# Optimization experiments

Hardware: AMD Instinct MI355X
Metric: run time of the kernel (lower is better)

## Reference

```python
import jax, jax.numpy as jnp
import numpy as np

B, S, D, H, DH, W, V, K = 2, 4096, 768, 12, 64, 128, 50265, 128
NEG = -1e9


def _ln(x, g, b, eps=1e-5):
    m = jnp.mean(x, axis=-1, keepdims=True)
    v = jnp.var(x, axis=-1, keepdims=True)
    return (x - m) * jax.lax.rsqrt(v + eps) * g + b


def _split_heads(x):  # [B,S,D] -> [B,H,S,DH]
    return x.reshape(B, S, H, DH).transpose(0, 2, 1, 3)


def _windows(xc):  # [B,H,C,W,DH] -> [B,H,C,3W,DH] (prev/self/next chunk)
    xp = jnp.pad(xc, ((0, 0), (0, 0), (1, 1), (0, 0), (0, 0)))
    return jnp.concatenate([xp[:, :, :-2], xp[:, :, 1:-1], xp[:, :, 2:]], axis=3)


def _forward(sentences, start_pieces, end_pieces, labels,
             emb, pos, ln0_g, ln0_b, wq, bq, wk, bk, wv, bv, wo, bo,
             ln1_g, ln1_b, w1, b1, w2, b2, ln2_g, ln2_b, exemplars):
    C = S // W
    scale = 1.0 / np.sqrt(DH)
    am = sentences != 1  # pad token id is 1 (mask = sentence_tokens != 1)
    gidx = jnp.concatenate([start_pieces, end_pieces], axis=1)  # [B,2] global tokens
    G = gidx.shape[1]

    # embeddings
    x = _ln(emb[sentences] + pos[None], ln0_g, ln0_b)  # [B,S,D]

    # --- Longformer layer: sliding-window + global attention ---
    q = _split_heads(x @ wq + bq)
    k = _split_heads(x @ wk + bk)
    v = _split_heads(x @ wv + bv)

    qc = q.reshape(B, H, C, W, DH)
    kw = _windows(k.reshape(B, H, C, W, DH))  # [B,H,C,3W,DH]
    vw = _windows(v.reshape(B, H, C, W, DH))

    # banded local scores
    sb = jnp.einsum('bhcqd,bhckd->bhcqk', qc, kw) * scale  # [B,H,C,W,3W]
    qi = jnp.arange(W)[:, None]
    kj = jnp.arange(3 * W)[None, :]
    band = jnp.abs(kj - W - qi) <= W  # [W,3W]
    amc = jnp.pad(am.reshape(B, C, W), ((0, 0), (1, 1), (0, 0)))
    amw = jnp.concatenate([amc[:, :-2], amc[:, 1:-1], amc[:, 2:]], axis=2)  # [B,C,3W]
    mask = band[None, None, None] & amw[:, None, :, None, :]
    sb = jnp.where(mask, sb, NEG).reshape(B, H, S, 3 * W)

    # every token also attends to the G global tokens
    gk = jnp.take_along_axis(k, gidx[:, None, :, None], axis=2)  # [B,H,G,DH]
    gv = jnp.take_along_axis(v, gidx[:, None, :, None], axis=2)
    sg = jnp.einsum('bhsd,bhgd->bhsg', q, gk) * scale  # [B,H,S,G]

    p = jax.nn.softmax(jnp.concatenate([sb, sg], axis=-1), axis=-1)
    pb = p[..., :3 * W].reshape(B, H, C, W, 3 * W)
    pg = p[..., 3 * W:]
    o = jnp.einsum('bhcqk,bhckd->bhcqd', pb, vw).reshape(B, H, S, DH)
    o = o + jnp.einsum('bhsg,bhgd->bhsd', pg, gv)

    # global query tokens attend to everything
    qg = jnp.take_along_axis(q, gidx[:, None, :, None], axis=2)  # [B,H,G,DH]
    sgq = jnp.einsum('bhgd,bhsd->bhgs', qg, k) * scale
    sgq = jnp.where(am[:, None, None, :], sgq, NEG)
    og = jnp.einsum('bhgs,bhsd->bhgd', jax.nn.softmax(sgq, axis=-1), v)

    o = o.transpose(0, 2, 1, 3).reshape(B, S, D)
    og = og.transpose(0, 2, 1, 3).reshape(B, G, D)
    o = o.at[jnp.arange(B)[:, None], gidx].set(og)

    x = _ln(x + (o @ wo + bo), ln1_g, ln1_b)
    ff = jax.nn.gelu(x @ w1 + b1, approximate=False) @ w2 + b2
    h = _ln(x + ff, ln2_g, ln2_b)  # last_hidden_state

    # mention reps: gather start & end piece vectors, concat -> [B, 2D]
    sv = jnp.take_along_axis(h, start_pieces[:, :, None], axis=1)[:, 0]
    ev = jnp.take_along_axis(h, end_pieces[:, :, None], axis=1)[:, 0]
    mention = jnp.concatenate([sv, ev], axis=-1)  # [B, 1536]

    logits = mention @ exemplars.T  # [B, K]
    logp = jax.nn.log_softmax(logits, axis=-1)
    loss = -jnp.sum(jnp.take_along_axis(logp, labels[:, None], axis=1))
    return logits, loss


def setup_inputs() -> dict:
    key = jax.random.key(0)
    ks = jax.random.split(key, 16)
    f = lambda k, s: (jax.random.normal(k, s, dtype=jnp.float32) * 0.02)
    return {
        'sentences': jax.random.randint(ks[0], (B, S), 0, V, dtype=jnp.int32),
        'start_pieces': jax.random.randint(ks[1], (B, 1), 0, S, dtype=jnp.int32),
        'end_pieces': jax.random.randint(ks[2], (B, 1), 0, S, dtype=jnp.int32),
        'labels': jax.random.randint(ks[3], (B,), 0, K, dtype=jnp.int32),
        'emb': f(ks[4], (V, D)), 'pos': f(ks[5], (S, D)),
        'ln0_g': jnp.ones(D), 'ln0_b': jnp.zeros(D),
        'wq': f(ks[6], (D, D)), 'bq': jnp.zeros(D),
        'wk': f(ks[7], (D, D)), 'bk': jnp.zeros(D),
        'wv': f(ks[8], (D, D)), 'bv': jnp.zeros(D),
        'wo': f(ks[9], (D, D)), 'bo': jnp.zeros(D),
        'ln1_g': jnp.ones(D), 'ln1_b': jnp.zeros(D),
        'w1': f(ks[10], (D, 4 * D)), 'b1': jnp.zeros(4 * D),
        'w2': f(ks[11], (4 * D, D)), 'b2': jnp.zeros(D),
        'ln2_g': jnp.ones(D), 'ln2_b': jnp.zeros(D),
        'exemplars': f(ks[12], (K, 2 * D)),
    }


def reference(sentences, start_pieces, end_pieces, labels,
              emb, pos, ln0_g, ln0_b, wq, bq, wk, bk, wv, bv, wo, bo,
              ln1_g, ln1_b, w1, b1, w2, b2, ln2_g, ln2_b, exemplars):
    return _forward(sentences, start_pieces, end_pieces, labels,
                    emb, pos, ln0_g, ln0_b, wq, bq, wk, bk, wv, bv, wo, bo,
                    ln1_g, ln1_b, w1, b1, w2, b2, ln2_g, ln2_b, exemplars)
```

## Files before the change

### kernel.cpp

```cpp
#include <hip/hip_runtime.h>

typedef unsigned short u16;
typedef unsigned int   u32;
typedef __attribute__((ext_vector_type(8))) short bf16x8;
typedef __attribute__((ext_vector_type(4))) float f32x4;

#define BB 2
#define SS 4096
#define DD 768
#define HH 12
#define FF 3072
#define NTOK 8192

#define GLDS16(gp, lp) __builtin_amdgcn_global_load_lds(                      \
    (const __attribute__((address_space(1))) u32*)(gp),                       \
    (__attribute__((address_space(3))) u32*)(lp), 16, 0, 0)

__device__ __forceinline__ float bf2f(u16 u) {
  u32 x = ((u32)u) << 16;
  return __uint_as_float(x);
}
__device__ __forceinline__ u16 f2bf(float f) {
  u32 x = __float_as_uint(f);
  x = x + 0x7FFFu + ((x >> 16) & 1u);
  return (u16)(x >> 16);
}
__device__ __forceinline__ float gelu_f(float v) {
  return 0.5f * v * (1.0f + erff(v * 0.70710678118654752f));
}

template<bool MAXOP>
__device__ __forceinline__ float blk_reduce(float v, float* sbuf) {
  #pragma unroll
  for (int o = 32; o > 0; o >>= 1) {
    float t = __shfl_xor(v, o, 64);
    v = MAXOP ? fmaxf(v, t) : (v + t);
  }
  int wave = threadIdx.x >> 6;
  int nw = blockDim.x >> 6;
  __syncthreads();
  if ((threadIdx.x & 63) == 0) sbuf[wave] = v;
  __syncthreads();
  float r = sbuf[0];
  for (int i = 1; i < nw; i++) r = MAXOP ? fmaxf(r, sbuf[i]) : (r + sbuf[i]);
  return r;
}

__global__ __launch_bounds__(256) void transcvt2(const float* __restrict__ wk,
    const float* __restrict__ wv, u16* __restrict__ wkT, u16* __restrict__ wvT) {
  const float* W = blockIdx.z ? wv : wk;
  u16* WT = blockIdx.z ? wvT : wkT;
  __shared__ float t[32][33];
  int n0 = blockIdx.x * 32, k0 = blockIdx.y * 32;
  int tx = threadIdx.x & 31, ty = threadIdx.x >> 5;
  #pragma unroll
  for (int i = 0; i < 32; i += 8)
    t[ty + i][tx] = W[(size_t)(k0 + ty + i) * DD + n0 + tx];
  __syncthreads();
  #pragma unroll
  for (int i = 0; i < 32; i += 8)
    WT[(size_t)(n0 + ty + i) * DD + k0 + tx] = f2bf(t[tx][ty + i]);
}

__global__ void seed_k(const int* sp, const int* ep, const float* bq, const float* bo,
                       const float* b1, const float* b2,
                       float* qg, float* oa, float* f1, float* f2, int* gidx) {
  int tid = threadIdx.x;
  if (tid < 4) {
    int b = tid >> 1;
    int s = (tid & 1) ? ep[b] : sp[b];
    gidx[tid] = b * SS + s;
  }
  for (int i = tid; i < DD; i += 256) {
    float vq = bq[i], vo = bo[i], v2 = b2[i];
    #pragma unroll
    for (int r = 0; r < 4; r++) {
      qg[r * DD + i] = vq; oa[r * DD + i] = vo; f2[r * DD + i] = v2;
    }
  }
  for (int i = tid; i < FF; i += 256) {
    float v1 = b1[i];
    #pragma unroll
    for (int r = 0; r < 4; r++) f1[r * FF + i] = v1;
  }
}

__global__ __launch_bounds__(192) void embed_ln_k(const int* __restrict__ sent,
    const float* __restrict__ emb, const float* __restrict__ pos,
    const float* __restrict__ g, const float* __restrict__ be, u16* __restrict__ xout) {
  __shared__ float sbuf[8];
  int tok = blockIdx.x;
  int s = tok & (SS - 1);
  int row = sent[tok];
  int tid = threadIdx.x;
  float4 e = *(const float4*)(emb + (size_t)row * DD + tid * 4);
  float4 p = *(const float4*)(pos + (size_t)s * DD + tid * 4);
  float v0 = e.x + p.x, v1 = e.y + p.y, v2 = e.z + p.z, v3 = e.w + p.w;
  float sum = v0 + v1 + v2 + v3;
  float sq  = v0 * v0 + v1 * v1 + v2 * v2 + v3 * v3;
  sum = blk_reduce<false>(sum, sbuf);
  sq  = blk_reduce<false>(sq, sbuf);
  float mean = sum * (1.f / DD);
  float var  = sq * (1.f / DD) - mean * mean;
  float rstd = rsqrtf(var + 1e-5f);
  float4 gg = *(const float4*)(g + tid * 4);
  float4 bb = *(const float4*)(be + tid * 4);
  float o0 = (v0 - mean) * rstd * gg.x + bb.x;
  float o1 = (v1 - mean) * rstd * gg.y + bb.y;
  float o2 = (v2 - mean) * rstd * gg.z + bb.z;
  float o3 = (v3 - mean) * rstd * gg.w + bb.w;
  u32 lo = (u32)f2bf(o0) | ((u32)f2bf(o1) << 16);
  u32 hi = (u32)f2bf(o2) | ((u32)f2bf(o3) << 16);
  uint2 st; st.x = lo; st.y = hi;
  *(uint2*)(xout + (size_t)tok * DD + tid * 4) = st;
}

__global__ __launch_bounds__(256) void gemm_kv(const u16* __restrict__ A,
    const u16* __restrict__ wkT, const u16* __restrict__ wvT,
    const float* __restrict__ bkp, const float* __restrict__ bvp,
    u16* __restrict__ kb, u16* __restrict__ vb) {
  const int K = DD, N = DD;
  __shared__ u16 As[128 * 32];
  __shared__ u16 Bs[128 * 32];
  int which = blockIdx.y >= 6;
  int m0 = blockIdx.x * 128;
  int n0 = (blockIdx.y - (which ? 6 : 0)) * 128;
  const u16* Bt = which ? wvT : wkT;
  const float* bias = which ? bvp : bkp;
  u16* C = which ? vb : kb;
  int tid = threadIdx.x;
  int lane = tid & 63, wave = tid >> 6;
  int wr = wave >> 1, wc = wave & 1;
  f32x4 acc[4][4] = {};
  int ch0 = wave * 64 + lane;
  int r0 = ch0 >> 2, su0 = ch0 & 3;
  int ch1 = 256 + ch0;
  int r1 = ch1 >> 2, su1 = ch1 & 3;
  const u16* a0p = A  + (size_t)(m0 + r0) * K + su0 * 8;
  const u16* a1p = A  + (size_t)(m0 + r1) * K + su1 * 8;
  const u16* b0p = Bt + (size_t)(n0 + r0) * K + su0 * 8;
  const u16* b1p = Bt + (size_t)(n0 + r1) * K + su1 * 8;
  u16* AsW0 = As + (size_t)(wave * 64) * 8;
  u16* AsW1 = As + (size_t)(256 + wave * 64) * 8;
  u16* BsW0 = Bs + (size_t)(wave * 64) * 8;
  u16* BsW1 = Bs + (size_t)(256 + wave * 64) * 8;
  int fr = lane & 15, fk = (lane >> 4) * 8;
  for (int k0 = 0; k0 < K; k0 += 32) {
    GLDS16(a0p + k0, AsW0);
    GLDS16(a1p + k0, AsW1);
    GLDS16(b0p + k0, BsW0);
    GLDS16(b1p + k0, BsW1);
    __syncthreads();
    bf16x8 af[4], bfr[4];
    #pragma unroll
    for (int i = 0; i < 4; i++)
      af[i] = *(const bf16x8*)(As + ((wr * 64 + i * 16 + fr) << 5) + fk);
    #pragma unroll
    for (int j = 0; j < 4; j++)
      bfr[j] = *(const bf16x8*)(Bs + ((wc * 64 + j * 16 + fr) << 5) + fk);
    #pragma unroll
    for (int i = 0; i < 4; i++)
      #pragma unroll
      for (int j = 0; j < 4; j++)
        acc[i][j] = __builtin_amdgcn_mfma_f32_16x16x32_bf16(af[i], bfr[j], acc[i][j], 0, 0, 0);
    __syncthreads();
  }
  int cr = (lane >> 4) * 4;
  int cc = lane & 15;
  #pragma unroll
  for (int i = 0; i < 4; i++) {
    #pragma unroll
    for (int j = 0; j < 4; j++) {
      int col = n0 + wc * 64 + j * 16 + cc;
      float bvv = bias[col];
      int rowb = m0 + wr * 64 + i * 16 + cr;
      #pragma unroll
      for (int r = 0; r < 4; r++) {
        float v = acc[i][j][r] + bvv;
        C[(size_t)(rowb + r) * N + col] = f2bf(v);
      }
    }
  }
}

__global__ __launch_bounds__(256) void matvec4(const float* __restrict__ W,
    const float* __restrict__ inF, const u16* __restrict__ inB, const int* __restrict__ gidx,
    float* __restrict__ acc, int K, int N, int kchunk, int mode) {
  __shared__ float s_in[4 * 256];
  int n = blockIdx.x * 256 + threadIdx.x;
  int k0 = blockIdx.y * kchunk;
  for (int idx = threadIdx.x; idx < 4 * kchunk; idx += 256) {
    int r = idx / kchunk, kk = idx - r * kchunk;
    float vv;
    if (mode == 1) vv = bf2f(inB[(size_t)gidx[r] * K + k0 + kk]);
    else vv = inF[(size_t)r * K + k0 + kk];
    if (mode == 2) vv = gelu_f(vv);
    s_in[r * 256 + kk] = vv;
  }
  __syncthreads();
  float a0 = 0.f, a1 = 0.f, a2 = 0.f, a3 = 0.f;
  for (int kk = 0; kk < kchunk; kk++) {
    float w = W[(size_t)(k0 + kk) * N + n];
    a0 += s_in[kk] * w;
    a1 += s_in[256 + kk] * w;
    a2 += s_in[512 + kk] * w;
    a3 += s_in[768 + kk] * w;
  }
  atomicAdd(&acc[n], a0);
  atomicAdd(&acc[N + n], a1);
  atomicAdd(&acc[2 * N + n], a2);
  atomicAdd(&acc[3 * N + n], a3);
}

__global__ __launch_bounds__(256) void gattn_part(const u16* __restrict__ kb,
    const u16* __restrict__ vb, const float* __restrict__ qg, const int* __restrict__ sent,
    float* __restrict__ part) {
  int sc = blockIdx.x, h = blockIdx.y, bg = blockIdx.z;
  int b = bg >> 1;
  __shared__ float pbuf[256];
  __shared__ float ovs[32][64];
  __shared__ float sbuf[8];
  int tid = threadIdx.x;
  int rsub = tid >> 3, csub = tid & 7;
  float qr[8];
  #pragma unroll
  for (int j = 0; j < 8; j++) qr[j] = qg[bg * DD + h * 64 + csub * 8 + j];
  size_t kbase = ((size_t)b * SS + sc * 256) * DD + h * 64 + csub * 8;
  #pragma unroll
  for (int pass = 0; pass < 8; pass++) {
    int rowi = pass * 32 + rsub;
    uint4 u = *(const uint4*)(kb + kbase + (size_t)rowi * DD);
    u32 vals[4] = {u.x, u.y, u.z, u.w};
    float dot = 0.f;
    #pragma unroll
    for (int t = 0; t < 4; t++) {
      dot += qr[t * 2]     * __uint_as_float(vals[t] << 16);
      dot += qr[t * 2 + 1] * __uint_as_float(vals[t] & 0xFFFF0000u);
    }
    dot += __shfl_xor(dot, 1, 64);
    dot += __shfl_xor(dot, 2, 64);
    dot += __shfl_xor(dot, 4, 64);
    if (csub == 0) pbuf[rowi] = dot;
  }
  __syncthreads();
  float score = (sent[b * SS + sc * 256 + tid] != 1) ? pbuf[tid] * 0.125f : -1e9f;
  float m = blk_reduce<true>(score, sbuf);
  float p = expf(score - m);
  float psum = blk_reduce<false>(p, sbuf);
  pbuf[tid] = p;
  __syncthreads();
  float a[8] = {0.f, 0.f, 0.f, 0.f, 0.f, 0.f, 0.f, 0.f};
  #pragma unroll
  for (int pass = 0; pass < 8; pass++) {
    int rowi = pass * 32 + rsub;
    uint4 u = *(const uint4*)(vb + kbase + (size_t)rowi * DD);
    u32 vals[4] = {u.x, u.y, u.z, u.w};
    float pw = pbuf[rowi];
    #pragma unroll
    for (int t = 0; t < 4; t++) {
      a[t * 2]     += pw * __uint_as_float(vals[t] << 16);
      a[t * 2 + 1] += pw * __uint_as_float(vals[t] & 0xFFFF0000u);
    }
  }
  #pragma unroll
  for (int j = 0; j < 8; j++) ovs[rsub][csub * 8 + j] = a[j];
  __syncthreads();
  float* pp = part + (((size_t)bg * HH + h) * 16 + sc) * 66;
  if (tid == 0) { pp[0] = m; pp[1] = psum; }
  if (tid < 64) {
    float o = 0.f;
    #pragma unroll
    for (int g2 = 0; g2 < 32; g2++) o += ovs[g2][tid];
    pp[2 + tid] = o;
  }
}

__global__ __launch_bounds__(256) void matvec_wo(const float* __restrict__ W,
    const float* __restrict__ part, float* __restrict__ acc) {
  __shared__ float s_in[4][64];
  int h = blockIdx.y;
  int tid = threadIdx.x;
  int bg = tid >> 6, d = tid & 63;
  const float* pp = part + (((size_t)bg * HH + h) * 16) * 66;
  float M = -1e30f;
  for (int c = 0; c < 16; c++) M = fmaxf(M, pp[c * 66]);
  float Ssum = 0.f, o = 0.f;
  for (int c = 0; c < 16; c++) {
    float e = expf(pp[c * 66] - M);
    Ssum += pp[c * 66 + 1] * e;
    o += pp[c * 66 + 2 + d] * e;
  }
  s_in[bg][d] = o / Ssum;
  __syncthreads();
  int n = blockIdx.x * 256 + tid;
  int k0 = h * 64;
  float a0 = 0.f, a1 = 0.f, a2 = 0.f, a3 = 0.f;
  for (int kk = 0; kk < 64; kk++) {
    float w = W[(size_t)(k0 + kk) * DD + n];
    a0 += s_in[0][kk] * w;
    a1 += s_in[1][kk] * w;
    a2 += s_in[2][kk] * w;
    a3 += s_in[3][kk] * w;
  }
  atomicAdd(&acc[n], a0);
  atomicAdd(&acc[DD + n], a1);
  atomicAdd(&acc[2 * DD + n], a2);
  atomicAdd(&acc[3 * DD + n], a3);
}

__global__ __launch_bounds__(256) void ln4_k(const u16* __restrict__ xb, const int* __restrict__ gidx,
    const float* __restrict__ in1f, const float* __restrict__ in2,
    const float* __restrict__ g, const float* __restrict__ be, float* __restrict__ outp) {
  __shared__ float sbuf[8];
  int r = blockIdx.x;
  float v[3];
  float sum = 0.f, sq = 0.f;
  #pragma unroll
  for (int i = 0; i < 3; i++) {
    int d = threadIdx.x + i * 256;
    float t;
    if (xb) t = bf2f(xb[(size_t)gidx[r] * DD + d]);
    else    t = in1f[r * DD + d];
    t += in2[r * DD + d];
    v[i] = t; sum += t; sq += t * t;
  }
  sum = blk_reduce<false>(sum, sbuf);
  sq  = blk_reduce<false>(sq, sbuf);
  float mean = sum * (1.f / DD);
  float var  = sq * (1.f / DD) - mean * mean;
  float rstd = rsqrtf(var + 1e-5f);
  #pragma unroll
  for (int i = 0; i < 3; i++) {
    int d = threadIdx.x + i * 256;
    outp[r * DD + d] = (v[i] - mean) * rstd * g[d] + be[d];
  }
}

__global__ __launch_bounds__(256) void logits_k(const float* __restrict__ hws,
    const float* __restrict__ ex, float* __restrict__ out) {
  __shared__ float sbuf[8];
  int j = blockIdx.x;
  const float* er = ex + (size_t)j * 1536;
  float d0 = 0.f, d1 = 0.f;
  for (int c = threadIdx.x; c < 768; c += 256) {
    float e0 = er[c], e1 = er[768 + c];
    d0 += hws[c] * e0 + hws[768 + c] * e1;
    d1 += hws[1536 + c] * e0 + hws[2304 + c] * e1;
  }
  d0 = blk_reduce<false>(d0, sbuf);
  d1 = blk_reduce<false>(d1, sbuf);
  if (threadIdx.x == 0) { out[j] = d0; out[128 + j] = d1; }
}

__global__ __launch_bounds__(128) void loss_k(const float* __restrict__ lg,
    const int* __restrict__ labels, float* __restrict__ out) {
  __shared__ float sbuf[8];
  int tid = threadIdx.x;
  float v0 = lg[tid], v1 = lg[128 + tid];
  float m0 = blk_reduce<true>(v0, sbuf);
  float m1 = blk_reduce<true>(v1, sbuf);
  float s0 = blk_reduce<false>(expf(v0 - m0), sbuf);
  float s1 = blk_reduce<false>(expf(v1 - m1), sbuf);
  if (tid == 0) {
    float lp0 = lg[labels[0]] - m0 - logf(s0);
    float lp1 = lg[128 + labels[1]] - m1 - logf(s1);
    out[256] = -(lp0 + lp1);
  }
}

extern "C" void kernel_launch(void* const* d_in, const int* in_sizes, int n_in,
                              void* d_out, int out_size, void* d_ws, size_t ws_size,
                              hipStream_t stream) {
  const int*   sent = (const int*)d_in[0];
  const int*   sp   = (const int*)d_in[1];
  const int*   ep   = (const int*)d_in[2];
  const int*   lab  = (const int*)d_in[3];
  const float* emb  = (const float*)d_in[4];
  const float* pos  = (const float*)d_in[5];
  const float* ln0g = (const float*)d_in[6];
  const float* ln0b = (const float*)d_in[7];
  const float* wq   = (const float*)d_in[8];
  const float* bq   = (const float*)d_in[9];
  const float* wk   = (const float*)d_in[10];
  const float* bk   = (const float*)d_in[11];
  const float* wv   = (const float*)d_in[12];
  const float* bv   = (const float*)d_in[13];
  const float* wo   = (const float*)d_in[14];
  const float* bo   = (const float*)d_in[15];
  const float* ln1g = (const float*)d_in[16];
  const float* ln1b = (const float*)d_in[17];
  const float* w1   = (const float*)d_in[18];
  const float* b1   = (const float*)d_in[19];
  const float* w2   = (const float*)d_in[20];
  const float* b2   = (const float*)d_in[21];
  const float* ln2g = (const float*)d_in[22];
  const float* ln2b = (const float*)d_in[23];
  const float* ex   = (const float*)d_in[24];
  float* out = (float*)d_out;

  char* basep = (char*)d_ws;
  size_t off = 0;
  auto alloc = [&](size_t bytes) -> void* {
    void* p = basep + off;
    off = (off + bytes + 255) & ~(size_t)255;
    return p;
  };
  u16*   xb   = (u16*)alloc((size_t)NTOK * DD * 2);
  u16*   kb   = (u16*)alloc((size_t)NTOK * DD * 2);
  u16*   vb   = (u16*)alloc((size_t)NTOK * DD * 2);
  u16*   wkT  = (u16*)alloc((size_t)DD * DD * 2);
  u16*   wvT  = (u16*)alloc((size_t)DD * DD * 2);
  float* qg   = (float*)alloc(4 * DD * 4);
  float* oacc = (float*)alloc(4 * DD * 4);
  float* x1   = (float*)alloc(4 * DD * 4);
  float* f1a  = (float*)alloc(4 * FF * 4);
  float* f2a  = (float*)alloc(4 * DD * 4);
  float* hws  = (float*)alloc(4 * DD * 4);
  float* part = (float*)alloc((size_t)4 * HH * 16 * 66 * 4);
  int*   gidx = (int*)alloc(64);

  transcvt2<<<dim3(24, 24, 2), 256, 0, stream>>>(wk, wv, wkT, wvT);
  seed_k<<<1, 256, 0, stream>>>(sp, ep, bq, bo, b1, b2, qg, oacc, f1a, f2a, gidx);
  embed_ln_k<<<NTOK, 192, 0, stream>>>(sent, emb, pos, ln0g, ln0b, xb);
  gemm_kv<<<dim3(64, 12), 256, 0, stream>>>(xb, wkT, wvT, bk, bv, kb, vb);
  matvec4<<<dim3(3, 12), 256, 0, stream>>>(wq, nullptr, xb, gidx, qg, DD, DD, 64, 1);
  gattn_part<<<dim3(16, HH, 4), 256, 0, stream>>>(kb, vb, qg, sent, part);
  matvec_wo<<<dim3(3, 12), 256, 0, stream>>>(wo, part, oacc);
  ln4_k<<<4, 256, 0, stream>>>(xb, gidx, nullptr, oacc, ln1g, ln1b, x1);
  matvec4<<<dim3(12, 12), 256, 0, stream>>>(w1, x1, nullptr, nullptr, f1a, DD, FF, 64, 0);
  matvec4<<<dim3(3, 24), 256, 0, stream>>>(w2, f1a, nullptr, nullptr, f2a, FF, DD, 128, 2);
  ln4_k<<<4, 256, 0, stream>>>(nullptr, nullptr, x1, f2a, ln2g, ln2b, hws);
  logits_k<<<128, 256, 0, stream>>>(hws, ex, out);
  loss_k<<<1, 128, 0, stream>>>(out, lab, out);
}
```

Baseline: 112.3 us.

## Fuse tail matvecs into cooperative kernel and merge small launches

Folds the seed kernel into the weight transpose kernel and the Wq matvec into the K/V GEMM launch, with an XCD-aware remapping of block ids. The attention-partials kernel now handles both global queries of a batch in one block, so each K/V chunk is read once instead of twice. The whole tail (Wo, LN1, FFN1, FFN2, LN2, logits, loss) becomes one cooperative kernel separated by grid syncs. This removes many small launches and their gaps, at the cost of grid-sync overhead and a fixed 192-block grid.

Measured after the change: 335.5 us. 199% more time.

```diff
diff --git a/kernel.cpp b/kernel.cpp
--- a/kernel.cpp
+++ b/kernel.cpp
@@ -1,4 +1,7 @@
 #include <hip/hip_runtime.h>
+#include <hip/hip_cooperative_groups.h>
+
+namespace cg = cooperative_groups;
 
 typedef unsigned short u16;
 typedef unsigned int   u32;
@@ -47,12 +50,35 @@
 }
 
 __global__ __launch_bounds__(256) void transcvt2(const float* __restrict__ wk,
-    const float* __restrict__ wv, u16* __restrict__ wkT, u16* __restrict__ wvT) {
+    const float* __restrict__ wv, u16* __restrict__ wkT, u16* __restrict__ wvT,
+    const int* sp, const int* ep, const float* bq, const float* bo,
+    const float* b1, const float* b2,
+    float* qg, float* oa, float* f1, float* f2, int* gidx) {
+  int tid = threadIdx.x;
+  if (blockIdx.x == 0 && blockIdx.y == 0 && blockIdx.z == 0) {
+    if (tid < 4) {
+      int b = tid >> 1;
+      int s = (tid & 1) ? ep[b] : sp[b];
+      gidx[tid] = b * SS + s;
+    }
+    for (int i = tid; i < DD; i += 256) {
+      float vq = bq[i], vo = bo[i], v2 = b2[i];
+      #pragma unroll
+      for (int r = 0; r < 4; r++) {
+        qg[r * DD + i] = vq; oa[r * DD + i] = vo; f2[r * DD + i] = v2;
+      }
+    }
+    for (int i = tid; i < FF; i += 256) {
+      float v1 = b1[i];
+      #pragma unroll
+      for (int r = 0; r < 4; r++) f1[r * FF + i] = v1;
+    }
+  }
   const float* W = blockIdx.z ? wv : wk;
   u16* WT = blockIdx.z ? wvT : wkT;
   __shared__ float t[32][33];
   int n0 = blockIdx.x * 32, k0 = blockIdx.y * 32;
-  int tx = threadIdx.x & 31, ty = threadIdx.x >> 5;
+  int tx = tid & 31, ty = tid >> 5;
   #pragma unroll
   for (int i = 0; i < 32; i += 8)
     t[ty + i][tx] = W[(size_t)(k0 + ty + i) * DD + n0 + tx];
@@ -60,29 +86,6 @@
   #pragma unroll
   for (int i = 0; i < 32; i += 8)
     WT[(size_t)(n0 + ty + i) * DD + k0 + tx] = f2bf(t[tx][ty + i]);
-}
-
-__global__ void seed_k(const int* sp, const int* ep, const float* bq, const float* bo,
-                       const float* b1, const float* b2,
-                       float* qg, float* oa, float* f1, float* f2, int* gidx) {
-  int tid = threadIdx.x;
-  if (tid < 4) {
-    int b = tid >> 1;
-    int s = (tid & 1) ? ep[b] : sp[b];
-    gidx[tid] = b * SS + s;
-  }
-  for (int i = tid; i < DD; i += 256) {
-    float vq = bq[i], vo = bo[i], v2 = b2[i];
-    #pragma unroll
-    for (int r = 0; r < 4; r++) {
-      qg[r * DD + i] = vq; oa[r * DD + i] = vo; f2[r * DD + i] = v2;
-    }
-  }
-  for (int i = tid; i < FF; i += 256) {
-    float v1 = b1[i];
-    #pragma unroll
-    for (int r = 0; r < 4; r++) f1[r * FF + i] = v1;
-  }
 }
 
 __global__ __launch_bounds__(192) void embed_ln_k(const int* __restrict__ sent,
@@ -118,17 +121,48 @@
 __global__ __launch_bounds__(256) void gemm_kv(const u16* __restrict__ A,
     const u16* __restrict__ wkT, const u16* __restrict__ wvT,
     const float* __restrict__ bkp, const float* __restrict__ bvp,
-    u16* __restrict__ kb, u16* __restrict__ vb) {
-  const int K = DD, N = DD;
+    u16* __restrict__ kb, u16* __restrict__ vb,
+    const float* __restrict__ wqw, const int* __restrict__ gidx,
+    float* __restrict__ qg) {
   __shared__ u16 As[128 * 32];
   __shared__ u16 Bs[128 * 32];
-  int which = blockIdx.y >= 6;
-  int m0 = blockIdx.x * 128;
-  int n0 = (blockIdx.y - (which ? 6 : 0)) * 128;
+  int orig = blockIdx.x;
+  int xcd = orig & 7, cidx = orig >> 3;
+  int wgid = (xcd < 4 ? xcd * 101 : 4 * 101 + (xcd - 4) * 100) + cidx;
+  int tid = threadIdx.x;
+  if (wgid >= 768) {
+    int wqi = wgid - 768;
+    int nc = wqi % 3, ky = wqi / 3;
+    float* s_in = (float*)As;
+    if (tid < 256) {
+      int rr = tid >> 6, kk = tid & 63;
+      s_in[tid] = bf2f(A[(size_t)gidx[rr] * DD + ky * 64 + kk]);
+    }
+    __syncthreads();
+    int n = nc * 256 + tid;
+    int k0 = ky * 64;
+    float a0 = 0.f, a1 = 0.f, a2 = 0.f, a3 = 0.f;
+    for (int kk = 0; kk < 64; kk++) {
+      float w = wqw[(size_t)(k0 + kk) * DD + n];
+      a0 += s_in[kk] * w;
+      a1 += s_in[64 + kk] * w;
+      a2 += s_in[128 + kk] * w;
+      a3 += s_in[192 + kk] * w;
+    }
+    atomicAdd(&qg[n], a0);
+    atomicAdd(&qg[DD + n], a1);
+    atomicAdd(&qg[2 * DD + n], a2);
+    atomicAdd(&qg[3 * DD + n], a3);
+    return;
+  }
+  const int K = DD, N = DD;
+  int mx = wgid / 12, t = wgid % 12;
+  int which = t >= 6;
+  int m0 = mx * 128;
+  int n0 = (t - (which ? 6 : 0)) * 128;
   const u16* Bt = which ? wvT : wkT;
   const float* bias = which ? bvp : bkp;
   u16* C = which ? vb : kb;
-  int tid = threadIdx.x;
   int lane = tid & 63, wave = tid >> 6;
   int wr = wave >> 1, wc = wave & 1;
   f32x4 acc[4][4] = {};
@@ -183,188 +217,251 @@
   }
 }
 
-__global__ __launch_bounds__(256) void matvec4(const float* __restrict__ W,
-    const float* __restrict__ inF, const u16* __restrict__ inB, const int* __restrict__ gidx,
-    float* __restrict__ acc, int K, int N, int kchunk, int mode) {
-  __shared__ float s_in[4 * 256];
-  int n = blockIdx.x * 256 + threadIdx.x;
-  int k0 = blockIdx.y * kchunk;
-  for (int idx = threadIdx.x; idx < 4 * kchunk; idx += 256) {
-    int r = idx / kchunk, kk = idx - r * kchunk;
-    float vv;
-    if (mode == 1) vv = bf2f(inB[(size_t)gidx[r] * K + k0 + kk]);
-    else vv = inF[(size_t)r * K + k0 + kk];
-    if (mode == 2) vv = gelu_f(vv);
-    s_in[r * 256 + kk] = vv;
-  }
-  __syncthreads();
-  float a0 = 0.f, a1 = 0.f, a2 = 0.f, a3 = 0.f;
-  for (int kk = 0; kk < kchunk; kk++) {
-    float w = W[(size_t)(k0 + kk) * N + n];
-    a0 += s_in[kk] * w;
-    a1 += s_in[256 + kk] * w;
-    a2 += s_in[512 + kk] * w;
-    a3 += s_in[768 + kk] * w;
-  }
-  atomicAdd(&acc[n], a0);
-  atomicAdd(&acc[N + n], a1);
-  atomicAdd(&acc[2 * N + n], a2);
-  atomicAdd(&acc[3 * N + n], a3);
-}
-
 __global__ __launch_bounds__(256) void gattn_part(const u16* __restrict__ kb,
     const u16* __restrict__ vb, const float* __restrict__ qg, const int* __restrict__ sent,
     float* __restrict__ part) {
-  int sc = blockIdx.x, h = blockIdx.y, bg = blockIdx.z;
-  int b = bg >> 1;
-  __shared__ float pbuf[256];
-  __shared__ float ovs[32][64];
+  int sc = blockIdx.x, h = blockIdx.y, b = blockIdx.z;
+  __shared__ float pbuf0[256], pbuf1[256];
+  __shared__ float ovs0[32][64], ovs1[32][64];
   __shared__ float sbuf[8];
   int tid = threadIdx.x;
   int rsub = tid >> 3, csub = tid & 7;
-  float qr[8];
-  #pragma unroll
-  for (int j = 0; j < 8; j++) qr[j] = qg[bg * DD + h * 64 + csub * 8 + j];
+  float qr0[8], qr1[8];
+  #pragma unroll
+  for (int j = 0; j < 8; j++) {
+    qr0[j] = qg[(2 * b) * DD + h * 64 + csub * 8 + j];
+    qr1[j] = qg[(2 * b + 1) * DD + h * 64 + csub * 8 + j];
+  }
   size_t kbase = ((size_t)b * SS + sc * 256) * DD + h * 64 + csub * 8;
   #pragma unroll
   for (int pass = 0; pass < 8; pass++) {
     int rowi = pass * 32 + rsub;
     uint4 u = *(const uint4*)(kb + kbase + (size_t)rowi * DD);
     u32 vals[4] = {u.x, u.y, u.z, u.w};
-    float dot = 0.f;
+    float d0 = 0.f, d1 = 0.f;
     #pragma unroll
     for (int t = 0; t < 4; t++) {
-      dot += qr[t * 2]     * __uint_as_float(vals[t] << 16);
-      dot += qr[t * 2 + 1] * __uint_as_float(vals[t] & 0xFFFF0000u);
-    }
-    dot += __shfl_xor(dot, 1, 64);
-    dot += __shfl_xor(dot, 2, 64);
-    dot += __shfl_xor(dot, 4, 64);
-    if (csub == 0) pbuf[rowi] = dot;
+      float lo = __uint_as_float(vals[t] << 16);
+      float hi = __uint_as_float(vals[t] & 0xFFFF0000u);
+      d0 += qr0[t * 2] * lo + qr0[t * 2 + 1] * hi;
+      d1 += qr1[t * 2] * lo + qr1[t * 2 + 1] * hi;
+    }
+    d0 += __shfl_xor(d0, 1, 64); d1 += __shfl_xor(d1, 1, 64);
+    d0 += __shfl_xor(d0, 2, 64); d1 += __shfl_xor(d1, 2, 64);
+    d0 += __shfl_xor(d0, 4, 64); d1 += __shfl_xor(d1, 4, 64);
+    if (csub == 0) { pbuf0[rowi] = d0; pbuf1[rowi] = d1; }
   }
   __syncthreads();
-  float score = (sent[b * SS + sc * 256 + tid] != 1) ? pbuf[tid] * 0.125f : -1e9f;
-  float m = blk_reduce<true>(score, sbuf);
-  float p = expf(score - m);
-  float psum = blk_reduce<false>(p, sbuf);
-  pbuf[tid] = p;
+  int ok = sent[b * SS + sc * 256 + tid] != 1;
+  float s0 = ok ? pbuf0[tid] * 0.125f : -1e9f;
+  float s1 = ok ? pbuf1[tid] * 0.125f : -1e9f;
+  float m0 = blk_reduce<true>(s0, sbuf);
+  float m1 = blk_reduce<true>(s1, sbuf);
+  float p0 = expf(s0 - m0);
+  float p1 = expf(s1 - m1);
+  float ps0 = blk_reduce<false>(p0, sbuf);
+  float ps1 = blk_reduce<false>(p1, sbuf);
+  pbuf0[tid] = p0;
+  pbuf1[tid] = p1;
   __syncthreads();
-  float a[8] = {0.f, 0.f, 0.f, 0.f, 0.f, 0.f, 0.f, 0.f};
+  float a0[8] = {0,0,0,0,0,0,0,0}, a1[8] = {0,0,0,0,0,0,0,0};
   #pragma unroll
   for (int pass = 0; pass < 8; pass++) {
     int rowi = pass * 32 + rsub;
     uint4 u = *(const uint4*)(vb + kbase + (size_t)rowi * DD);
     u32 vals[4] = {u.x, u.y, u.z, u.w};
-    float pw = pbuf[rowi];
+    float pw0 = pbuf0[rowi], pw1 = pbuf1[rowi];
     #pragma unroll
     for (int t = 0; t < 4; t++) {
-      a[t * 2]     += pw * __uint_as_float(vals[t] << 16);
-      a[t * 2 + 1] += pw * __uint_as_float(vals[t] & 0xFFFF0000u);
-    }
-  }
-  #pragma unroll
-  for (int j = 0; j < 8; j++) ovs[rsub][csub * 8 + j] = a[j];
+      float lo = __uint_as_float(vals[t] << 16);
+      float hi = __uint_as_float(vals[t] & 0xFFFF0000u);
+      a0[t * 2]     += pw0 * lo; a0[t * 2 + 1] += pw0 * hi;
+      a1[t * 2]     += pw1 * lo; a1[t * 2 + 1] += pw1 * hi;
+    }
+  }
+  #pragma unroll
+  for (int j = 0; j < 8; j++) {
+    ovs0[rsub][csub * 8 + j] = a0[j];
+    ovs1[rsub][csub * 8 + j] = a1[j];
+  }
   __syncthreads();
-  float* pp = part + (((size_t)bg * HH + h) * 16 + sc) * 66;
-  if (tid == 0) { pp[0] = m; pp[1] = psum; }
+  float* pp0 = part + (((size_t)(2 * b) * HH + h) * 16 + sc) * 66;
+  float* pp1 = part + (((size_t)(2 * b + 1) * HH + h) * 16 + sc) * 66;
+  if (tid == 0) { pp0[0] = m0; pp0[1] = ps0; pp1[0] = m1; pp1[1] = ps1; }
   if (tid < 64) {
-    float o = 0.f;
-    #pragma unroll
-    for (int g2 = 0; g2 < 32; g2++) o += ovs[g2][tid];
-    pp[2 + tid] = o;
-  }
-}
-
-__global__ __launch_bounds__(256) void matvec_wo(const float* __restrict__ W,
-    const float* __restrict__ part, float* __restrict__ acc) {
-  __shared__ float s_in[4][64];
-  int h = blockIdx.y;
-  int tid = threadIdx.x;
-  int bg = tid >> 6, d = tid & 63;
-  const float* pp = part + (((size_t)bg * HH + h) * 16) * 66;
-  float M = -1e30f;
-  for (int c = 0; c < 16; c++) M = fmaxf(M, pp[c * 66]);
-  float Ssum = 0.f, o = 0.f;
-  for (int c = 0; c < 16; c++) {
-    float e = expf(pp[c * 66] - M);
-    Ssum += pp[c * 66 + 1] * e;
-    o += pp[c * 66 + 2 + d] * e;
-  }
-  s_in[bg][d] = o / Ssum;
-  __syncthreads();
-  int n = blockIdx.x * 256 + tid;
-  int k0 = h * 64;
-  float a0 = 0.f, a1 = 0.f, a2 = 0.f, a3 = 0.f;
-  for (int kk = 0; kk < 64; kk++) {
-    float w = W[(size_t)(k0 + kk) * DD + n];
-    a0 += s_in[0][kk] * w;
-    a1 += s_in[1][kk] * w;
-    a2 += s_in[2][kk] * w;
-    a3 += s_in[3][kk] * w;
-  }
-  atomicAdd(&acc[n], a0);
-  atomicAdd(&acc[DD + n], a1);
-  atomicAdd(&acc[2 * DD + n], a2);
-  atomicAdd(&acc[3 * DD + n], a3);
-}
-
-__global__ __launch_bounds__(256) void ln4_k(const u16* __restrict__ xb, const int* __restrict__ gidx,
-    const float* __restrict__ in1f, const float* __restrict__ in2,
-    const float* __restrict__ g, const float* __restrict__ be, float* __restrict__ outp) {
+    float o0 = 0.f, o1 = 0.f;
+    #pragma unroll
+    for (int g2 = 0; g2 < 32; g2++) { o0 += ovs0[g2][tid]; o1 += ovs1[g2][tid]; }
+    pp0[2 + tid] = o0;
+    pp1[2 + tid] = o1;
+  }
+}
+
+struct TailArgs {
+  const float* part; const float* wo; float* oacc;
+  const u16* xb; const int* gidx;
+  const float* ln1g; const float* ln1b; float* x1;
+  const float* w1; float* f1a;
+  const float* w2; float* f2a;
+  const float* ln2g; const float* ln2b; float* hws;
+  const float* ex; float* out; const int* lab;
+};
+
+__global__ __launch_bounds__(256) void tail_k(TailArgs a) {
+  cg::grid_group grid = cg::this_grid();
+  int blk = blockIdx.x, tid = threadIdx.x;
   __shared__ float sbuf[8];
-  int r = blockIdx.x;
-  float v[3];
-  float sum = 0.f, sq = 0.f;
-  #pragma unroll
-  for (int i = 0; i < 3; i++) {
-    int d = threadIdx.x + i * 256;
-    float t;
-    if (xb) t = bf2f(xb[(size_t)gidx[r] * DD + d]);
-    else    t = in1f[r * DD + d];
-    t += in2[r * DD + d];
-    v[i] = t; sum += t; sq += t * t;
-  }
-  sum = blk_reduce<false>(sum, sbuf);
-  sq  = blk_reduce<false>(sq, sbuf);
-  float mean = sum * (1.f / DD);
-  float var  = sq * (1.f / DD) - mean * mean;
-  float rstd = rsqrtf(var + 1e-5f);
-  #pragma unroll
-  for (int i = 0; i < 3; i++) {
-    int d = threadIdx.x + i * 256;
-    outp[r * DD + d] = (v[i] - mean) * rstd * g[d] + be[d];
-  }
-}
-
-__global__ __launch_bounds__(256) void logits_k(const float* __restrict__ hws,
-    const float* __restrict__ ex, float* __restrict__ out) {
-  __shared__ float sbuf[8];
-  int j = blockIdx.x;
-  const float* er = ex + (size_t)j * 1536;
-  float d0 = 0.f, d1 = 0.f;
-  for (int c = threadIdx.x; c < 768; c += 256) {
-    float e0 = er[c], e1 = er[768 + c];
-    d0 += hws[c] * e0 + hws[768 + c] * e1;
-    d1 += hws[1536 + c] * e0 + hws[2304 + c] * e1;
-  }
-  d0 = blk_reduce<false>(d0, sbuf);
-  d1 = blk_reduce<false>(d1, sbuf);
-  if (threadIdx.x == 0) { out[j] = d0; out[128 + j] = d1; }
-}
-
-__global__ __launch_bounds__(128) void loss_k(const float* __restrict__ lg,
-    const int* __restrict__ labels, float* __restrict__ out) {
-  __shared__ float sbuf[8];
-  int tid = threadIdx.x;
-  float v0 = lg[tid], v1 = lg[128 + tid];
-  float m0 = blk_reduce<true>(v0, sbuf);
-  float m1 = blk_reduce<true>(v1, sbuf);
-  float s0 = blk_reduce<false>(expf(v0 - m0), sbuf);
-  float s1 = blk_reduce<false>(expf(v1 - m1), sbuf);
-  if (tid == 0) {
-    float lp0 = lg[labels[0]] - m0 - logf(s0);
-    float lp1 = lg[128 + labels[1]] - m1 - logf(s1);
-    out[256] = -(lp0 + lp1);
+  __shared__ float sm[4][64];
+  __shared__ float sin[192];
+  if (blk < 36) {
+    int nc = blk % 3, h = blk / 3;
+    int bg = tid >> 6, d = tid & 63;
+    const float* pp = a.part + ((size_t)(bg * HH + h) * 16) * 66;
+    float M = -1e30f;
+    for (int c = 0; c < 16; c++) M = fmaxf(M, pp[c * 66]);
+    float Ssum = 0.f, o = 0.f;
+    for (int c = 0; c < 16; c++) {
+      float e = expf(pp[c * 66] - M);
+      Ssum += pp[c * 66 + 1] * e;
+      o += pp[c * 66 + 2 + d] * e;
+    }
+    sm[bg][d] = o / Ssum;
+    __syncthreads();
+    int n = nc * 256 + tid;
+    float a0 = 0.f, a1 = 0.f, a2 = 0.f, a3 = 0.f;
+    for (int kk = 0; kk < 64; kk++) {
+      float w = a.wo[(size_t)(h * 64 + kk) * DD + n];
+      a0 += sm[0][kk] * w;
+      a1 += sm[1][kk] * w;
+      a2 += sm[2][kk] * w;
+      a3 += sm[3][kk] * w;
+    }
+    atomicAdd(&a.oacc[n], a0);
+    atomicAdd(&a.oacc[DD + n], a1);
+    atomicAdd(&a.oacc[2 * DD + n], a2);
+    atomicAdd(&a.oacc[3 * DD + n], a3);
+  }
+  __threadfence();
+  grid.sync();
+  if (blk < 4) {
+    float v[3]; float sum = 0.f, sq = 0.f;
+    #pragma unroll
+    for (int i = 0; i < 3; i++) {
+      int d = tid + i * 256;
+      float t = bf2f(a.xb[(size_t)a.gidx[blk] * DD + d]) + a.oacc[blk * DD + d];
+      v[i] = t; sum += t; sq += t * t;
+    }
+    sum = blk_reduce<false>(sum, sbuf);
+    sq  = blk_reduce<false>(sq, sbuf);
+    float mean = sum * (1.f / DD);
+    float rstd = rsqrtf(sq * (1.f / DD) - mean * mean + 1e-5f);
+    #pragma unroll
+    for (int i = 0; i < 3; i++) {
+      int d = tid + i * 256;
+      a.x1[blk * DD + d] = (v[i] - mean) * rstd * a.ln1g[d] + a.ln1b[d];
+    }
+  }
+  __threadfence();
+  grid.sync();
+  {
+    int nc = blk % 12, kc = blk / 12;
+    int k0 = kc * 48;
+    if (tid < 192) {
+      int rr = tid / 48, kk = tid - rr * 48;
+      sin[tid] = a.x1[rr * DD + k0 + kk];
+    }
+    __syncthreads();
+    int n = nc * 256 + tid;
+    float a0 = 0.f, a1 = 0.f, a2 = 0.f, a3 = 0.f;
+    for (int kk = 0; kk < 48; kk++) {
+      float w = a.w1[(size_t)(k0 + kk) * FF + n];
+      a0 += sin[kk] * w;
+      a1 += sin[48 + kk] * w;
+      a2 += sin[96 + kk] * w;
+      a3 += sin[144 + kk] * w;
+    }
+    atomicAdd(&a.f1a[n], a0);
+    atomicAdd(&a.f1a[FF + n], a1);
+    atomicAdd(&a.f1a[2 * FF + n], a2);
+    atomicAdd(&a.f1a[3 * FF + n], a3);
+  }
+  __threadfence();
+  grid.sync();
+  {
+    int nc = blk % 3, kc = blk / 3;
+    int k0 = kc * 48;
+    __syncthreads();
+    if (tid < 192) {
+      int rr = tid / 48, kk = tid - rr * 48;
+      sin[tid] = gelu_f(a.f1a[rr * FF + k0 + kk]);
+    }
+    __syncthreads();
+    int n = nc * 256 + tid;
+    float a0 = 0.f, a1 = 0.f, a2 = 0.f, a3 = 0.f;
+    for (int kk = 0; kk < 48; kk++) {
+      float w = a.w2[(size_t)(k0 + kk) * DD + n];
+      a0 += sin[kk] * w;
+      a1 += sin[48 + kk] * w;
+      a2 += sin[96 + kk] * w;
+      a3 += sin[144 + kk] * w;
+    }
+    atomicAdd(&a.f2a[n], a0);
+    atomicAdd(&a.f2a[DD + n], a1);
+    atomicAdd(&a.f2a[2 * DD + n], a2);
+    atomicAdd(&a.f2a[3 * DD + n], a3);
+  }
+  __threadfence();
+  grid.sync();
+  if (blk < 4) {
+    float v[3]; float sum = 0.f, sq = 0.f;
+    #pragma unroll
+    for (int i = 0; i < 3; i++) {
+      int d = tid + i * 256;
+      float t = a.x1[blk * DD + d] + a.f2a[blk * DD + d];
+      v[i] = t; sum += t; sq += t * t;
+    }
+    sum = blk_reduce<false>(sum, sbuf);
+    sq  = blk_reduce<false>(sq, sbuf);
+    float mean = sum * (1.f / DD);
+    float rstd = rsqrtf(sq * (1.f / DD) - mean * mean + 1e-5f);
+    #pragma unroll
+    for (int i = 0; i < 3; i++) {
+      int d = tid + i * 256;
+      a.hws[blk * DD + d] = (v[i] - mean) * rstd * a.ln2g[d] + a.ln2b[d];
+    }
+  }
+  __threadfence();
+  grid.sync();
+  if (blk < 128) {
+    int j = blk;
+    const float* er = a.ex + (size_t)j * 1536;
+    float d0 = 0.f, d1 = 0.f;
+    for (int c = tid; c < 768; c += 256) {
+      float e0 = er[c], e1 = er[768 + c];
+      d0 += a.hws[c] * e0 + a.hws[768 + c] * e1;
+      d1 += a.hws[1536 + c] * e0 + a.hws[2304 + c] * e1;
+    }
+    d0 = blk_reduce<false>(d0, sbuf);
+    d1 = blk_reduce<false>(d1, sbuf);
+    if (tid == 0) { a.out[j] = d0; a.out[128 + j] = d1; }
+  }
+  __threadfence();
+  grid.sync();
+  if (blk == 0) {
+    const float* lg = a.out;
+    float v0 = (tid < 128) ? lg[tid] : -3e38f;
+    float v1 = (tid < 128) ? lg[128 + tid] : -3e38f;
+    float m0 = blk_reduce<true>(v0, sbuf);
+    float m1 = blk_reduce<true>(v1, sbuf);
+    float e0 = (tid < 128) ? expf(v0 - m0) : 0.f;
+    float e1 = (tid < 128) ? expf(v1 - m1) : 0.f;
+    float s0 = blk_reduce<false>(e0, sbuf);
+    float s1 = blk_reduce<false>(e1, sbuf);
+    if (tid == 0) {
+      float lp0 = lg[a.lab[0]] - m0 - logf(s0);
+      float lp1 = lg[128 + a.lab[1]] - m1 - logf(s1);
+      a.out[256] = -(lp0 + lp1);
+    }
   }
 }
 
@@ -419,17 +516,20 @@
   float* part = (float*)alloc((size_t)4 * HH * 16 * 66 * 4);
   int*   gidx = (int*)alloc(64);
 
-  transcvt2<<<dim3(24, 24, 2), 256, 0, stream>>>(wk, wv, wkT, wvT);
-  seed_k<<<1, 256, 0, stream>>>(sp, ep, bq, bo, b1, b2, qg, oacc, f1a, f2a, gidx);
+  transcvt2<<<dim3(24, 24, 2), 256, 0, stream>>>(wk, wv, wkT, wvT,
+      sp, ep, bq, bo, b1, b2, qg, oacc, f1a, f2a, gidx);
   embed_ln_k<<<NTOK, 192, 0, stream>>>(sent, emb, pos, ln0g, ln0b, xb);
-  gemm_kv<<<dim3(64, 12), 256, 0, stream>>>(xb, wkT, wvT, bk, bv, kb, vb);
-  matvec4<<<dim3(3, 12), 256, 0, stream>>>(wq, nullptr, xb, gidx, qg, DD, DD, 64, 1);
-  gattn_part<<<dim3(16, HH, 4), 256, 0, stream>>>(kb, vb, qg, sent, part);
-  matvec_wo<<<dim3(3, 12), 256, 0, stream>>>(wo, part, oacc);
-  ln4_k<<<4, 256, 0, stream>>>(xb, gidx, nullptr, oacc, ln1g, ln1b, x1);
-  matvec4<<<dim3(12, 12), 256, 0, stream>>>(w1, x1, nullptr, nullptr, f1a, DD, FF, 64, 0);
-  matvec4<<<dim3(3, 24), 256, 0, stream>>>(w2, f1a, nullptr, nullptr, f2a, FF, DD, 128, 2);
-  ln4_k<<<4, 256, 0, stream>>>(nullptr, nullptr, x1, f2a, ln2g, ln2b, hws);
-  logits_k<<<128, 256, 0, stream>>>(hws, ex, out);
-  loss_k<<<1, 128, 0, stream>>>(out, lab, out);
-}
+  gemm_kv<<<804, 256, 0, stream>>>(xb, wkT, wvT, bk, bv, kb, vb, wq, gidx, qg);
+  gattn_part<<<dim3(16, HH, 2), 256, 0, stream>>>(kb, vb, qg, sent, part);
+
+  TailArgs ta;
+  ta.part = part; ta.wo = wo; ta.oacc = oacc;
+  ta.xb = xb; ta.gidx = gidx;
+  ta.ln1g = ln1g; ta.ln1b = ln1b; ta.x1 = x1;
+  ta.w1 = w1; ta.f1a = f1a;
+  ta.w2 = w2; ta.f2a = f2a;
+  ta.ln2g = ln2g; ta.ln2b = ln2b; ta.hws = hws;
+  ta.ex = ex; ta.out = out; ta.lab = lab;
+  void* kargs[] = { &ta };
+  hipLaunchCooperativeKernel((const void*)tail_k, dim3(192), dim3(256), kargs, 0, stream);
+}
```
